# Optimization experiments

Hardware: AMD Instinct MI355X
Metric: run time of the kernel (lower is better)

## Reference

```python
import jax, jax.numpy as jnp
import numpy as np


def setup_inputs() -> dict:
    key = jax.random.key(0)
    k1, k2, k3, k4, k5 = jax.random.split(key, 5)
    B, S, Q = 64, 2048, 512
    query = jax.random.normal(k1, (1, B, Q), dtype=jnp.float32)
    projected_memory = jax.random.normal(k2, (B, S, Q), dtype=jnp.float32)
    mask = jax.random.randint(k3, (B, S), 0, 2, dtype=jnp.int32)
    Wq = jax.random.normal(k4, (Q, Q), dtype=jnp.float32) * (1.0 / np.sqrt(Q))
    We = jax.random.normal(k5, (Q,), dtype=jnp.float32) * (1.0 / np.sqrt(Q))
    return {"query": query, "projected_memory": projected_memory, "mask": mask,
            "Wq": Wq, "We": We}


def reference(query, projected_memory, mask, Wq, We):
    # query: [1, B, Q]; nn.Linear applies x @ W.T
    proj_query = jnp.einsum('tbq,dq->tbd', query, Wq)          # [1, B, Q]
    proj_query = jnp.transpose(proj_query, (1, 0, 2))          # [B, 1, Q]
    energy = jnp.tanh(proj_query + projected_memory)           # [B, S, Q]
    energy = jnp.einsum('bsq,q->bs', energy, We)               # [B, S]
    energy = jnp.where(mask == 0, jnp.float32(-1000.0), energy)
    attn = jax.nn.softmax(energy, axis=1)                      # [B, S]
    return attn[:, None, :]                                    # [B, 1, S]
```

## Files before the change

### kernel.cpp

```cpp
#include <hip/hip_runtime.h>

constexpr int B_ = 64;
constexpr int S_ = 2048;
constexpr int Q_ = 512;

constexpr int PARTIAL_OFF = B_ * Q_;

__device__ __forceinline__ float tanh_fast(float x) {
  float e = __expf(2.0f * x);
  float r = __builtin_amdgcn_rcpf(e + 1.0f);
  return fmaf(-2.0f, r, 1.0f);
}

__device__ __forceinline__ float wave_reduce_sum(float v) {
#pragma unroll
  for (int off = 32; off > 0; off >>= 1) v += __shfl_xor(v, off, 64);
  return v;
}

__global__ __launch_bounds__(256) void proj_kernel(const float* __restrict__ query,
                                                   const float* __restrict__ Wq,
                                                   float* __restrict__ pq) {
  int wave = threadIdx.x >> 6, lane = threadIdx.x & 63;
  int w = blockIdx.x * 4 + wave;
  int b = w >> 7;
  int d0 = (w & 127) * 4;
  int q0 = lane * 4, q1 = 256 + lane * 4;
  float4 qa = *(const float4*)(query + b * Q_ + q0);
  float4 qb = *(const float4*)(query + b * Q_ + q1);
#pragma unroll
  for (int j = 0; j < 4; ++j) {
    const float* wrow = Wq + (long long)(d0 + j) * Q_;
    float4 wa = *(const float4*)(wrow + q0);
    float4 wb = *(const float4*)(wrow + q1);
    float acc = qa.x * wa.x + qa.y * wa.y + qa.z * wa.z + qa.w * wa.w +
                qb.x * wb.x + qb.y * wb.y + qb.z * wb.z + qb.w * wb.w;
    acc = wave_reduce_sum(acc);
    if (lane == 0) pq[b * Q_ + d0 + j] = acc;
  }
}

__global__ __launch_bounds__(256) void energy_kernel(const float* __restrict__ pm,
                                                     const int* __restrict__ mask,
                                                     const float* __restrict__ pq,
                                                     const float* __restrict__ We,
                                                     float* __restrict__ p_out,
                                                     float* __restrict__ partial) {
  int wave = threadIdx.x >> 6, lane = threadIdx.x & 63;
  int w = blockIdx.x * 4 + wave;
  int b = w >> 8;
  int s0 = (w & 255) * 8;
  int q0 = lane * 4, q1 = 256 + lane * 4;

  const float* pqrow = pq + b * Q_;
  float4 pa = *(const float4*)(pqrow + q0);
  float4 pb = *(const float4*)(pqrow + q1);
  float4 wa = *(const float4*)(We + q0);
  float4 wb = *(const float4*)(We + q1);

  const float* pmb = pm + ((long long)b * S_ + s0) * Q_;
  const int* mrow = mask + b * S_ + s0;
  float* erow = p_out + b * S_ + s0;

  float expsum = 0.0f;
#pragma unroll
  for (int r = 0; r < 8; ++r) {
    if (mrow[r] == 0) {
      if (lane == 0) erow[r] = 0.0f;
      continue;
    }
    const float* prow = pmb + (long long)r * Q_;
    float4 ma = *(const float4*)(prow + q0);
    float4 mb = *(const float4*)(prow + q1);
    float acc = wa.x * tanh_fast(pa.x + ma.x);
    acc = fmaf(wa.y, tanh_fast(pa.y + ma.y), acc);
    acc = fmaf(wa.z, tanh_fast(pa.z + ma.z), acc);
    acc = fmaf(wa.w, tanh_fast(pa.w + ma.w), acc);
    acc = fmaf(wb.x, tanh_fast(pb.x + mb.x), acc);
    acc = fmaf(wb.y, tanh_fast(pb.y + mb.y), acc);
    acc = fmaf(wb.z, tanh_fast(pb.z + mb.z), acc);
    acc = fmaf(wb.w, tanh_fast(pb.w + mb.w), acc);
    acc = wave_reduce_sum(acc);
    float e = __expf(acc);
    expsum += e;
    if (lane == 0) erow[r] = e;
  }

  __shared__ float wsum[4];
  if (lane == 0) wsum[wave] = expsum;
  __syncthreads();
  if (threadIdx.x == 0)
    partial[blockIdx.x] = (wsum[0] + wsum[1]) + (wsum[2] + wsum[3]);
}

__global__ __launch_bounds__(256) void scale_kernel(float* __restrict__ p,
                                                    const float* __restrict__ partial) {
  int b = blockIdx.x >> 2, c = blockIdx.x & 3;
  int lane = threadIdx.x & 63;
  float ps = partial[b * 64 + lane];
  ps = wave_reduce_sum(ps);
  float inv = 1.0f / ps;
  float2* row = (float2*)(p + b * S_ + c * 512) + threadIdx.x;
  float2 v = *row;
  v.x *= inv;
  v.y *= inv;
  *row = v;
}

extern "C" void kernel_launch(void* const* d_in, const int* in_sizes, int n_in,
                              void* d_out, int out_size, void* d_ws, size_t ws_size,
                              hipStream_t stream) {
  const float* query = (const float*)d_in[0];
  const float* pm    = (const float*)d_in[1];
  const int*   mask  = (const int*)d_in[2];
  const float* Wq    = (const float*)d_in[3];
  const float* We    = (const float*)d_in[4];
  float* out     = (float*)d_out;
  float* pq      = (float*)d_ws;
  float* partial = (float*)d_ws + PARTIAL_OFF;

  proj_kernel<<<2048, 256, 0, stream>>>(query, Wq, pq);
  energy_kernel<<<4096, 256, 0, stream>>>(pm, mask, pq, We, out, partial);
  scale_kernel<<<256, 256, 0, stream>>>(out, partial);
}
```

Before: 35.65 us.

## Batch masked row loads and interleave wave reductions in energy kernel

Loads the 8 mask values as two int4 vectors into a bitmask. It then issues all eight rows' projected_memory loads up front, before any compute, so more memory requests are in flight per wave. The eight row dot products are reduced together with interleaved shuffles, and the exps are written as two float4 stores. Masked rows now get an accumulator of -1000 (-1000/64 per lane summed across the wave) and are exponentiated rather than written as zero. This matches the reference masking, at the cost of higher register pressure.

```diff
diff --git a/kernel.cpp b/kernel.cpp
--- a/kernel.cpp
+++ b/kernel.cpp
@@ -59,33 +59,67 @@
   float4 wb = *(const float4*)(We + q1);
 
   const float* pmb = pm + ((long long)b * S_ + s0) * Q_;
-  const int* mrow = mask + b * S_ + s0;
   float* erow = p_out + b * S_ + s0;
 
-  float expsum = 0.0f;
+  const int4* m4 = (const int4*)(mask + b * S_ + s0);
+  int4 mlo = m4[0];
+  int4 mhi = m4[1];
+  unsigned bits = (mlo.x != 0 ? 1u : 0u) | (mlo.y != 0 ? 2u : 0u) |
+                  (mlo.z != 0 ? 4u : 0u) | (mlo.w != 0 ? 8u : 0u) |
+                  (mhi.x != 0 ? 16u : 0u) | (mhi.y != 0 ? 32u : 0u) |
+                  (mhi.z != 0 ? 64u : 0u) | (mhi.w != 0 ? 128u : 0u);
+
+  float4 a0x, a0y, a1x, a1y, a2x, a2y, a3x, a3y;
+  float4 a4x, a4y, a5x, a5y, a6x, a6y, a7x, a7y;
+#define LD(r)                                             \
+  if (bits & (1u << r)) {                                 \
+    const float* p_ = pmb + r * Q_;                       \
+    a##r##x = *(const float4*)(p_ + q0);                  \
+    a##r##y = *(const float4*)(p_ + q1);                  \
+  }
+  LD(0) LD(1) LD(2) LD(3) LD(4) LD(5) LD(6) LD(7)
+#undef LD
+
+  constexpr float MINIT = -1000.0f / 64.0f;
+  float acc0 = MINIT, acc1 = MINIT, acc2 = MINIT, acc3 = MINIT;
+  float acc4 = MINIT, acc5 = MINIT, acc6 = MINIT, acc7 = MINIT;
+#define DOT(r)                                            \
+  if (bits & (1u << r)) {                                 \
+    float t = wa.x * tanh_fast(pa.x + a##r##x.x);         \
+    t = fmaf(wa.y, tanh_fast(pa.y + a##r##x.y), t);       \
+    t = fmaf(wa.z, tanh_fast(pa.z + a##r##x.z), t);       \
+    t = fmaf(wa.w, tanh_fast(pa.w + a##r##x.w), t);       \
+    t = fmaf(wb.x, tanh_fast(pb.x + a##r##y.x), t);       \
+    t = fmaf(wb.y, tanh_fast(pb.y + a##r##y.y), t);       \
+    t = fmaf(wb.z, tanh_fast(pb.z + a##r##y.z), t);       \
+    t = fmaf(wb.w, tanh_fast(pb.w + a##r##y.w), t);       \
+    acc##r = t;                                           \
+  }
+  DOT(0) DOT(1) DOT(2) DOT(3) DOT(4) DOT(5) DOT(6) DOT(7)
+#undef DOT
+
 #pragma unroll
-  for (int r = 0; r < 8; ++r) {
-    if (mrow[r] == 0) {
-      if (lane == 0) erow[r] = 0.0f;
-      continue;
-    }
-    const float* prow = pmb + (long long)r * Q_;
-    float4 ma = *(const float4*)(prow + q0);
-    float4 mb = *(const float4*)(prow + q1);
-    float acc = wa.x * tanh_fast(pa.x + ma.x);
-    acc = fmaf(wa.y, tanh_fast(pa.y + ma.y), acc);
-    acc = fmaf(wa.z, tanh_fast(pa.z + ma.z), acc);
-    acc = fmaf(wa.w, tanh_fast(pa.w + ma.w), acc);
-    acc = fmaf(wb.x, tanh_fast(pb.x + mb.x), acc);
-    acc = fmaf(wb.y, tanh_fast(pb.y + mb.y), acc);
-    acc = fmaf(wb.z, tanh_fast(pb.z + mb.z), acc);
-    acc = fmaf(wb.w, tanh_fast(pb.w + mb.w), acc);
-    acc = wave_reduce_sum(acc);
-    float e = __expf(acc);
-    expsum += e;
-    if (lane == 0) erow[r] = e;
+  for (int off = 32; off > 0; off >>= 1) {
+    acc0 += __shfl_xor(acc0, off, 64);
+    acc1 += __shfl_xor(acc1, off, 64);
+    acc2 += __shfl_xor(acc2, off, 64);
+    acc3 += __shfl_xor(acc3, off, 64);
+    acc4 += __shfl_xor(acc4, off, 64);
+    acc5 += __shfl_xor(acc5, off, 64);
+    acc6 += __shfl_xor(acc6, off, 64);
+    acc7 += __shfl_xor(acc7, off, 64);
+  }
+  float e0 = __expf(acc0), e1 = __expf(acc1), e2 = __expf(acc2), e3 = __expf(acc3);
+  float e4 = __expf(acc4), e5 = __expf(acc5), e6 = __expf(acc6), e7 = __expf(acc7);
+
+  if (lane == 0) {
+    float4 o0 = {e0, e1, e2, e3};
+    float4 o1 = {e4, e5, e6, e7};
+    *(float4*)erow = o0;
+    *(float4*)(erow + 4) = o1;
   }
 
+  float expsum = ((e0 + e1) + (e2 + e3)) + ((e4 + e5) + (e6 + e7));
   __shared__ float wsum[4];
   if (lane == 0) wsum[wave] = expsum;
   __syncthreads();
```

After: 33.99 us. 1.05x faster.
